# Optimization experiments

Measured on AMD Instinct MI355X. Metric: run time of the kernel, lower is better.

The kernel has to match this reference:

```python
import jax, jax.numpy as jnp
import numpy as np

B, S = 2048, 512
VOCAB, MAXPOS = 50000, 512
DE = 50          # each embedding dim; concat -> 100
DIN, H, OUT = 100, 512, 2


def setup_inputs() -> dict:
    key = jax.random.key(0)
    ks = jax.random.split(key, 12)
    inp = {
        "emb_table": jax.random.normal(ks[0], (VOCAB, DE), jnp.float32) * 0.02,
        "pos_table": jax.random.normal(ks[1], (MAXPOS, DE), jnp.float32) * 0.02,
        "W1": jax.random.normal(ks[2], (DIN, H), jnp.float32) / np.sqrt(DIN),
        "b1": jnp.zeros((H,), jnp.float32),
        "W2": jax.random.normal(ks[3], (H, H), jnp.float32) / np.sqrt(H),
        "b2": jnp.zeros((H,), jnp.float32),
        "W3": jax.random.normal(ks[4], (H, H), jnp.float32) / np.sqrt(H),
        "b3": jnp.zeros((H,), jnp.float32),
        "Wf": jax.random.normal(ks[5], (H, OUT), jnp.float32) / np.sqrt(H),
        "bf": jnp.zeros((OUT,), jnp.float32),
        "seq": jax.random.randint(ks[6], (B, S), 0, VOCAB),
        "seq_length": jax.random.randint(ks[7], (B,), 1, S + 1),  # >=1 to avoid div-by-zero, as in real data
        "pos": jnp.tile(jnp.arange(S, dtype=jnp.int64 if jax.config.jax_enable_x64 else jnp.int32)[None, :], (B, 1)),
    }
    return inp


def reference(emb_table, pos_table, W1, b1, W2, b2, W3, b3, Wf, bf,
              seq, seq_length, pos):
    # Embedding lookups + concat on feature dim -> [B, S, 100]
    x = jnp.concatenate([emb_table[seq], pos_table[pos]], axis=2)
    # Masked mean over the first seq_length[i] tokens (replaces the Python double loop)
    mask = (jnp.arange(S)[None, :] < seq_length[:, None]).astype(x.dtype)  # [B, S]
    pooled = jnp.einsum("bsd,bs->bd", x, mask) / seq_length[:, None].astype(x.dtype)  # [B, 100]
    # MLP stack (Dropout p=0.5 is identity in eval mode)
    h = jax.nn.relu(pooled @ W1 + b1)
    h = jax.nn.relu(h @ W2 + b2)
    h = jax.nn.relu(h @ W3 + b3)
    return h @ Wf + bf  # [B, OUT]
```

## Files before the change

kernel.cpp:

```cpp
#include <hip/hip_runtime.h>

typedef __attribute__((ext_vector_type(8))) short bf16x8;
typedef __attribute__((ext_vector_type(4))) float f32x4;

#define B_    2048
#define S_    512

#define OFF_WF1   0u
#define OFF_WF2   131072u
#define OFF_WF3   655360u
#define OFF_WFF   1179648u
#define OFF_PREF  1196032u
#define OFF_EMBB  1327104u
#define WS_NEED   (OFF_EMBB + 6400000u)

__device__ __forceinline__ unsigned short f2bf(float f) {
    unsigned int u = __float_as_uint(f);
    u += 0x7FFFu + ((u >> 16) & 1u);
    return (unsigned short)(u >> 16);
}

#define MFMA16(a, b, c) __builtin_amdgcn_mfma_f32_16x16x32_bf16((a), (b), (c), 0, 0, 0)

__global__ __launch_bounds__(256) void prep_convert(
    const float* __restrict__ W1, const float* __restrict__ W2,
    const float* __restrict__ W3, const float* __restrict__ Wf,
    const float* __restrict__ post, const int* __restrict__ pos,
    const float* __restrict__ emb,
    unsigned short* __restrict__ ws, float* __restrict__ pref, int do_emb)
{
    const int bid = blockIdx.x;
    const int tid = threadIdx.x;

    if (bid < 152) {
        __shared__ float tile[64][65];
        const float* src; unsigned short* dst;
        int k0, n0, Ksrc, Nsrc, ksTot, nTiles;
        if (bid < 64)       { src=W2; dst=ws+OFF_WF2/2; k0=(bid>>3)*64; n0=(bid&7)*64; Ksrc=512; Nsrc=512; ksTot=16; nTiles=4; }
        else if (bid < 128) { int b=bid-64;  src=W3; dst=ws+OFF_WF3/2; k0=(b>>3)*64; n0=(b&7)*64; Ksrc=512; Nsrc=512; ksTot=16; nTiles=4; }
        else if (bid < 144) { int b=bid-128; src=W1; dst=ws+OFF_WF1/2; k0=(b>>3)*64; n0=(b&7)*64; Ksrc=100; Nsrc=512; ksTot=4;  nTiles=4; }
        else                { int b=bid-144; src=Wf; dst=ws+OFF_WFF/2; k0=b*64;      n0=0;        Ksrc=512; Nsrc=2;   ksTot=16; nTiles=1; }

        const int c  = tid & 63;
        const int r4 = tid >> 6;
#pragma unroll
        for (int rr = 0; rr < 16; ++rr) {
            int r = rr*4 + r4;
            float v = 0.f;
            if (k0 + r < Ksrc && n0 + c < Nsrc) v = src[(size_t)(k0+r)*Nsrc + n0 + c];
            tile[r][c] = v;
        }
        __syncthreads();
        const int nWords = nTiles * 2 * 64;
        for (int w = tid; w < nWords; w += 256) {
            int lane = w & 63, ks_l = (w >> 6) & 1, nt_l = w >> 7;
            int kr = ks_l*32 + ((lane >> 4) << 3);
            int nc = nt_l*16 + (lane & 15);
            uint4 wv;
            wv.x = (unsigned)f2bf(tile[kr+0][nc]) | ((unsigned)f2bf(tile[kr+1][nc]) << 16);
            wv.y = (unsigned)f2bf(tile[kr+2][nc]) | ((unsigned)f2bf(tile[kr+3][nc]) << 16);
            wv.z = (unsigned)f2bf(tile[kr+4][nc]) | ((unsigned)f2bf(tile[kr+5][nc]) << 16);
            wv.w = (unsigned)f2bf(tile[kr+6][nc]) | ((unsigned)f2bf(tile[kr+7][nc]) << 16);
            int ntile = (n0 >> 4) + nt_l, ks = (k0 >> 5) + ks_l;
            ((uint4*)dst)[(size_t)(ntile*ksTot + ks)*64 + lane] = wv;
        }
    } else if (bid == 152) {
        __shared__ int   idx_s[512];
        __shared__ float csum[4][52];
        idx_s[tid]       = pos[tid];
        idx_s[tid + 256] = pos[tid + 256];
        __syncthreads();
        const int c = tid >> 6, d = tid & 63;
        if (d < 50) {
            float run = 0.f;
            for (int b8 = 0; b8 < 16; ++b8) {
                float t[8];
#pragma unroll
                for (int u = 0; u < 8; ++u)
                    t[u] = post[(size_t)idx_s[c*128 + b8*8 + u]*50 + d];
#pragma unroll
                for (int u = 0; u < 8; ++u) {
                    run += t[u];
                    pref[(size_t)(c*128 + b8*8 + u)*64 + d] = run;
                }
            }
            csum[c][d] = run;
        }
        __syncthreads();
        if (d < 50 && c > 0) {
            float off = 0.f;
            for (int cc = 0; cc < c; ++cc) off += csum[cc][d];
            for (int b8 = 0; b8 < 16; ++b8) {
                float t[8];
#pragma unroll
                for (int u = 0; u < 8; ++u)
                    t[u] = pref[(size_t)(c*128 + b8*8 + u)*64 + d];
#pragma unroll
                for (int u = 0; u < 8; ++u)
                    pref[(size_t)(c*128 + b8*8 + u)*64 + d] = t[u] + off;
            }
        }
    } else {
        if (!do_emb) return;
        unsigned* embw = (unsigned*)(ws + OFF_EMBB/2);
        const float2* e2 = (const float2*)emb;
        const unsigned q0 = (unsigned)(bid - 153) * 2048u + (unsigned)tid;
        float2 v[8];
#pragma unroll
        for (int u = 0; u < 8; ++u) {
            unsigned q = q0 + (unsigned)u*256u;
            v[u] = (q < 1250000u) ? e2[q] : (float2){0.f, 0.f};
        }
#pragma unroll
        for (int u = 0; u < 8; ++u) {
            unsigned q = q0 + (unsigned)u*256u;
            if (q < 1250000u) {
                unsigned r = q / 25u, c2 = q - r*25u;
                embw[(size_t)r*32u + c2] =
                    (unsigned)f2bf(v[u].x) | ((unsigned)f2bf(v[u].y) << 16);
            }
        }
    }
}

__device__ __forceinline__ void load_afrags(bf16x8 (&a)[16],
    const unsigned short* h, int row, int kq)
{
#pragma unroll
    for (int ks = 0; ks < 16; ++ks)
        a[ks] = *(const bf16x8*)((const char*)h +
                  (((unsigned)(row * 1024 + ks * 64 + kq * 16)) ^ ((row & 7) << 4)));
}

__device__ __forceinline__ void store_h(unsigned short* h, const f32x4 (&acc)[4],
    const float (&bb)[4], int wave, int row, int kq)
{
#pragma unroll
    for (int nt = 0; nt < 4; ++nt) {
        int c = wave*64 + nt*16 + row;
#pragma unroll
        for (int r4 = 0; r4 < 4; ++r4) {
            int hrow = kq*4 + r4;
            unsigned base = hrow * 1024;
            *(unsigned short*)((char*)h + ((base + c*2) ^ ((hrow & 7) << 4))) =
                f2bf(fmaxf(acc[nt][r4] + bb[nt], 0.f));
        }
    }
}

__device__ __forceinline__ void layer512(
    const bf16x8 (&a)[16], const unsigned short* __restrict__ Wfrag,
    const float* __restrict__ bias, unsigned short* hout,
    int wave, int row, int kq, int lane)
{
    const bf16x8* bp = (const bf16x8*)Wfrag + ((size_t)(wave*4) * 16 * 64) + lane;
    float bb[4];
#pragma unroll
    for (int nt = 0; nt < 4; ++nt) bb[nt] = bias[wave*64 + nt*16 + row];

    bf16x8 bvA[16], bvB[16];
#pragma unroll
    for (int ks = 0; ks < 16; ++ks) bvA[ks] = bp[(0*16 + ks)*64];
#pragma unroll
    for (int ks = 0; ks < 16; ++ks) bvB[ks] = bp[(1*16 + ks)*64];

    f32x4 acc[4];
    acc[0] = (f32x4){0.f,0.f,0.f,0.f};
#pragma unroll
    for (int ks = 0; ks < 16; ++ks) acc[0] = MFMA16(a[ks], bvA[ks], acc[0]);
#pragma unroll
    for (int ks = 0; ks < 16; ++ks) bvA[ks] = bp[(2*16 + ks)*64];

    acc[1] = (f32x4){0.f,0.f,0.f,0.f};
#pragma unroll
    for (int ks = 0; ks < 16; ++ks) acc[1] = MFMA16(a[ks], bvB[ks], acc[1]);
#pragma unroll
    for (int ks = 0; ks < 16; ++ks) bvB[ks] = bp[(3*16 + ks)*64];

    acc[2] = (f32x4){0.f,0.f,0.f,0.f};
#pragma unroll
    for (int ks = 0; ks < 16; ++ks) acc[2] = MFMA16(a[ks], bvA[ks], acc[2]);
    acc[3] = (f32x4){0.f,0.f,0.f,0.f};
#pragma unroll
    for (int ks = 0; ks < 16; ++ks) acc[3] = MFMA16(a[ks], bvB[ks], acc[3]);

    store_h(hout, acc, bb, wave, row, kq);
}

template<int EMODE>
__global__ __launch_bounds__(512, 2) void dan_fused(
    const float* __restrict__ emb, const int* __restrict__ seq,
    const int* __restrict__ seqlen, const unsigned short* __restrict__ ws_ro,
    const float* __restrict__ pref,
    const float* __restrict__ b1, const float* __restrict__ b2,
    const float* __restrict__ b3, const float* __restrict__ bfin,
    float* __restrict__ out)
{
    __shared__ __align__(16) unsigned short idx_s[8*512];
    __shared__ __align__(16) unsigned short pooled_s[16*144];
    __shared__ __align__(16) unsigned short hA[8192];
    __shared__ __align__(16) unsigned short hB[8192];

    const int tid  = threadIdx.x;
    const int wave = tid >> 6;
    const int lane = tid & 63;
    const int row  = lane & 15;
    const int kq   = lane >> 4;
    const int b0   = blockIdx.x * 8;

    const unsigned short* WF1 = ws_ro + OFF_WF1 / 2;
    const unsigned short* WF2 = ws_ro + OFF_WF2 / 2;
    const unsigned short* WF3 = ws_ro + OFF_WF3 / 2;
    const unsigned short* WFF = ws_ro + OFF_WFF / 2;

    for (int i = tid; i < 8*512; i += 512)
        idx_s[i] = (unsigned short)seq[(size_t)b0 * S_ + i];
    for (int i = tid; i < 16*144; i += 512) pooled_s[i] = 0;

    bf16x8 w1f[4][4];
    {
        const bf16x8* bp1 = (const bf16x8*)WF1 + ((size_t)(wave*4) * 4 * 64) + lane;
#pragma unroll
        for (int ci = 0; ci < 4; ++ci)
#pragma unroll
            for (int ks = 0; ks < 4; ++ks) w1f[ci][ks] = bp1[(ci*4 + ks)*64];
    }
    __syncthreads();

    const int L = seqlen[b0 + wave];
    const float Lf = (float)L;
    const unsigned short* idxr = idx_s + wave * 512;

    if (EMODE == 0) {
        const int tg = lane >> 3, dq = lane & 7;
        const uint4* tbl = (const uint4*)(ws_ro + OFF_EMBB / 2);
        float acc8[8];
#pragma unroll
        for (int j = 0; j < 8; ++j) acc8[j] = 0.f;

        const int Lfull = L & ~63;
        for (int s0 = 0; s0 < Lfull; s0 += 64) {
            uint4 q[8];
#pragma unroll
            for (int u = 0; u < 8; ++u) {
                int tok = idxr[s0 + u*8 + tg];
                q[u] = tbl[(size_t)tok * 8 + dq];
            }
#pragma unroll
            for (int u = 0; u < 8; ++u) {
                unsigned dw[4] = {q[u].x, q[u].y, q[u].z, q[u].w};
#pragma unroll
                for (int v = 0; v < 4; ++v) {
                    acc8[2*v]   += __uint_as_float(dw[v] << 16);
                    acc8[2*v+1] += __uint_as_float(dw[v] & 0xffff0000u);
                }
            }
        }
        for (int s0 = Lfull; s0 < L; s0 += 8) {
            int s = s0 + tg;
            uint4 q = {0u,0u,0u,0u};
            if (s < L) q = tbl[(size_t)idxr[s] * 8 + dq];
            unsigned dw[4] = {q.x, q.y, q.z, q.w};
#pragma unroll
            for (int v = 0; v < 4; ++v) {
                acc8[2*v]   += __uint_as_float(dw[v] << 16);
                acc8[2*v+1] += __uint_as_float(dw[v] & 0xffff0000u);
            }
        }
#pragma unroll
        for (int j = 0; j < 8; ++j) acc8[j] += __shfl_xor(acc8[j], 8);
#pragma unroll
        for (int j = 0; j < 8; ++j) acc8[j] += __shfl_xor(acc8[j], 16);
#pragma unroll
        for (int j = 0; j < 8; ++j) acc8[j] += __shfl_xor(acc8[j], 32);
        if (lane < 8) {
#pragma unroll
            for (int j = 0; j < 8; ++j) {
                int d = lane*8 + j;
                if (d < 50) pooled_s[wave*144 + d] = f2bf(acc8[j] / Lf);
            }
        }
    } else {
        float accE = 0.f;
        for (int s = 0; s < L; ++s) {
            int tok = idxr[s];
            if (lane < 50) accE += emb[(size_t)tok*50 + lane];
        }
        if (lane < 50) pooled_s[wave*144 + lane] = f2bf(accE / Lf);
    }
    if (lane < 50)
        pooled_s[wave*144 + 50 + lane] = f2bf(pref[(size_t)(L-1)*64 + lane] / Lf);
    __syncthreads();

    {
        bf16x8 a1[4];
#pragma unroll
        for (int ks = 0; ks < 4; ++ks)
            a1[ks] = *(const bf16x8*)&pooled_s[row*144 + ks*32 + kq*8];
        f32x4 acc[4];
        float bb[4];
#pragma unroll
        for (int ci = 0; ci < 4; ++ci) {
            bb[ci] = b1[wave*64 + ci*16 + row];
            acc[ci] = (f32x4){0.f,0.f,0.f,0.f};
#pragma unroll
            for (int ks = 0; ks < 4; ++ks) acc[ci] = MFMA16(a1[ks], w1f[ci][ks], acc[ci]);
        }
        store_h(hA, acc, bb, wave, row, kq);
    }
    __syncthreads();

    bf16x8 a[16];
    load_afrags(a, hA, row, kq);
    layer512(a, WF2, b2, hB, wave, row, kq, lane);
    __syncthreads();

    load_afrags(a, hB, row, kq);
    layer512(a, WF3, b3, hA, wave, row, kq, lane);
    __syncthreads();

    if (wave == 0) {
        load_afrags(a, hA, row, kq);
        const bf16x8* bpf = (const bf16x8*)WFF + lane;
        f32x4 accf = {0.f, 0.f, 0.f, 0.f};
#pragma unroll
        for (int ks = 0; ks < 16; ++ks) {
            bf16x8 bv = bpf[ks*64];
            accf = MFMA16(a[ks], bv, accf);
        }
        if (row < 2 && kq < 2) {
            float bb = bfin[row];
#pragma unroll
            for (int r4 = 0; r4 < 4; ++r4) {
                int m = kq*4 + r4;
                out[(size_t)(b0 + m) * 2 + row] = accf[r4] + bb;
            }
        }
    }
}

extern "C" void kernel_launch(void* const* d_in, const int* in_sizes, int n_in,
                              void* d_out, int out_size, void* d_ws, size_t ws_size,
                              hipStream_t stream)
{
    const float* emb    = (const float*)d_in[0];
    const float* post   = (const float*)d_in[1];
    const float* W1     = (const float*)d_in[2];
    const float* b1     = (const float*)d_in[3];
    const float* W2     = (const float*)d_in[4];
    const float* b2     = (const float*)d_in[5];
    const float* W3     = (const float*)d_in[6];
    const float* b3     = (const float*)d_in[7];
    const float* Wf     = (const float*)d_in[8];
    const float* bf     = (const float*)d_in[9];
    const int*   seq    = (const int*)d_in[10];
    const int*   seqlen = (const int*)d_in[11];
    const int*   pos    = (const int*)d_in[12];
    float*       out    = (float*)d_out;

    unsigned short* ws = (unsigned short*)d_ws;
    float* pref = (float*)((char*)d_ws + OFF_PREF);
    const int do_emb = (ws_size >= (size_t)WS_NEED) ? 1 : 0;

    const int prep_blocks = do_emb ? (153 + 611) : 153;
    prep_convert<<<prep_blocks, 256, 0, stream>>>(W1, W2, W3, Wf, post, pos, emb,
                                                  ws, pref, do_emb);
    if (do_emb)
        dan_fused<0><<<B_ / 8, 512, 0, stream>>>(emb, seq, seqlen, ws, pref,
                                                 b1, b2, b3, bf, out);
    else
        dan_fused<1><<<B_ / 8, 512, 0, stream>>>(emb, seq, seqlen, ws, pref,
                                                 b1, b2, b3, bf, out);
}
```

Before: 44.13 us.

## Split embedding pooling into its own kernel ahead of MLP kernel

Moves the gather-and-mean pooling out of the fused MLP kernel into a separate pool_kernel with 4 rows per 256-thread block (512 blocks), writing bf16 pooled rows to a global workspace buffer. The gather loop is rewritten as a software-pipelined loop that keeps four loads in flight, and the MLP kernel now only reads the pooled rows. The aim is to raise occupancy and memory-level parallelism for the latency-bound gather, which was previously limited by the heavy MLP kernel's resources and its per-block imbalance from varying sequence lengths. In exchange it adds an extra kernel launch and a global round trip for the pooled activations.

```diff
diff --git a/kernel.cpp b/kernel.cpp
--- a/kernel.cpp
+++ b/kernel.cpp
@@ -11,7 +11,8 @@
 #define OFF_WF3   655360u
 #define OFF_WFF   1179648u
 #define OFF_PREF  1196032u
-#define OFF_EMBB  1327104u
+#define OFF_POOLG 1327104u
+#define OFF_EMBB  1851392u
 #define WS_NEED   (OFF_EMBB + 6400000u)
 
 __device__ __forceinline__ unsigned short f2bf(float f) {
@@ -123,6 +124,88 @@
     }
 }
 
+__device__ __forceinline__ void acc_uint4(float (&a)[8], uint4 q) {
+    unsigned dw[4] = {q.x, q.y, q.z, q.w};
+#pragma unroll
+    for (int v = 0; v < 4; ++v) {
+        a[2*v]   += __uint_as_float(dw[v] << 16);
+        a[2*v+1] += __uint_as_float(dw[v] & 0xffff0000u);
+    }
+}
+
+#define LOADQ(qv, bidx) { int s_ = (bidx)*8 + tg; qv = (uint4){0u,0u,0u,0u}; \
+    if (s_ < L) qv = tbl[(size_t)idxr[s_]*8u + (unsigned)dq]; }
+
+template<int EMODE>
+__global__ __launch_bounds__(256) void pool_kernel(
+    const float* __restrict__ emb, const int* __restrict__ seq,
+    const int* __restrict__ seqlen, const unsigned short* __restrict__ ws_ro,
+    const float* __restrict__ pref, unsigned short* __restrict__ pooled_g)
+{
+    __shared__ unsigned short idx_s[4*512];
+    const int tid = threadIdx.x, wave = tid >> 6, lane = tid & 63;
+    const int b0 = blockIdx.x * 4;
+    for (int i = tid; i < 4*512; i += 256)
+        idx_s[i] = (unsigned short)seq[(size_t)b0 * S_ + i];
+    __syncthreads();
+
+    const int row = b0 + wave;
+    const int L = seqlen[row];
+    const float invL = 1.f / (float)L;
+    const unsigned short* idxr = idx_s + wave*512;
+
+    if (EMODE == 0) {
+        const int tg = lane >> 3, dq = lane & 7;
+        const uint4* tbl = (const uint4*)(ws_ro + OFF_EMBB/2);
+        float acc8[8] = {0.f,0.f,0.f,0.f,0.f,0.f,0.f,0.f};
+        uint4 q0, q1, q2, q3;
+        LOADQ(q0, 0) LOADQ(q1, 1) LOADQ(q2, 2) LOADQ(q3, 3)
+        const int nbr = (L + 7) >> 3;
+        for (int i = 0; i < nbr; i += 4) {
+            acc_uint4(acc8, q0); LOADQ(q0, i+4)
+            acc_uint4(acc8, q1); LOADQ(q1, i+5)
+            acc_uint4(acc8, q2); LOADQ(q2, i+6)
+            acc_uint4(acc8, q3); LOADQ(q3, i+7)
+        }
+#pragma unroll
+        for (int j = 0; j < 8; ++j) acc8[j] += __shfl_xor(acc8[j], 8);
+#pragma unroll
+        for (int j = 0; j < 8; ++j) acc8[j] += __shfl_xor(acc8[j], 16);
+#pragma unroll
+        for (int j = 0; j < 8; ++j) acc8[j] += __shfl_xor(acc8[j], 32);
+        if (lane < 16) {
+            const float* prow = pref + (size_t)(L-1)*64;
+            unsigned short w8[8];
+#pragma unroll
+            for (int j = 0; j < 8; ++j) {
+                int d = lane*8 + j;
+                float v;
+                if (d < 50)       v = acc8[j] * invL;
+                else if (d < 100) v = prow[d - 50] * invL;
+                else              v = 0.f;
+                w8[j] = f2bf(v);
+            }
+            bf16x8 wv;
+#pragma unroll
+            for (int j = 0; j < 8; ++j) wv[j] = (short)w8[j];
+            ((bf16x8*)pooled_g)[(size_t)row*16 + lane] = wv;
+        }
+    } else {
+        float accE = 0.f;
+        for (int s = 0; s < L; ++s) {
+            int tok = idxr[s];
+            if (lane < 50) accE += emb[(size_t)tok*50 + lane];
+        }
+        if (lane < 50)  pooled_g[(size_t)row*128 + lane] = f2bf(accE * invL);
+        else if (lane < 64) pooled_g[(size_t)row*128 + lane + 64] = 0;
+        if (lane < 50)
+            pooled_g[(size_t)row*128 + 50 + lane] =
+                f2bf(pref[(size_t)(L-1)*64 + lane] * invL);
+        else if (lane < 64)
+            pooled_g[(size_t)row*128 + (lane - 50 >= 0 ? 0 : 0) + 100 + (lane - 50)] = 0;
+    }
+}
+
 __device__ __forceinline__ void load_afrags(bf16x8 (&a)[16],
     const unsigned short* h, int row, int kq)
 {
@@ -187,16 +270,12 @@
     store_h(hout, acc, bb, wave, row, kq);
 }
 
-template<int EMODE>
-__global__ __launch_bounds__(512, 2) void dan_fused(
-    const float* __restrict__ emb, const int* __restrict__ seq,
-    const int* __restrict__ seqlen, const unsigned short* __restrict__ ws_ro,
-    const float* __restrict__ pref,
+__global__ __launch_bounds__(512, 2) void dan_mlp(
+    const unsigned short* __restrict__ ws_ro,
     const float* __restrict__ b1, const float* __restrict__ b2,
     const float* __restrict__ b3, const float* __restrict__ bfin,
     float* __restrict__ out)
 {
-    __shared__ __align__(16) unsigned short idx_s[8*512];
     __shared__ __align__(16) unsigned short pooled_s[16*144];
     __shared__ __align__(16) unsigned short hA[8192];
     __shared__ __align__(16) unsigned short hB[8192];
@@ -212,10 +291,7 @@
     const unsigned short* WF2 = ws_ro + OFF_WF2 / 2;
     const unsigned short* WF3 = ws_ro + OFF_WF3 / 2;
     const unsigned short* WFF = ws_ro + OFF_WFF / 2;
-
-    for (int i = tid; i < 8*512; i += 512)
-        idx_s[i] = (unsigned short)seq[(size_t)b0 * S_ + i];
-    for (int i = tid; i < 16*144; i += 512) pooled_s[i] = 0;
+    const unsigned short* pooled_g = ws_ro + OFF_POOLG / 2;
 
     bf16x8 w1f[4][4];
     {
@@ -225,71 +301,13 @@
 #pragma unroll
             for (int ks = 0; ks < 4; ++ks) w1f[ci][ks] = bp1[(ci*4 + ks)*64];
     }
-    __syncthreads();
-
-    const int L = seqlen[b0 + wave];
-    const float Lf = (float)L;
-    const unsigned short* idxr = idx_s + wave * 512;
-
-    if (EMODE == 0) {
-        const int tg = lane >> 3, dq = lane & 7;
-        const uint4* tbl = (const uint4*)(ws_ro + OFF_EMBB / 2);
-        float acc8[8];
-#pragma unroll
-        for (int j = 0; j < 8; ++j) acc8[j] = 0.f;
-
-        const int Lfull = L & ~63;
-        for (int s0 = 0; s0 < Lfull; s0 += 64) {
-            uint4 q[8];
-#pragma unroll
-            for (int u = 0; u < 8; ++u) {
-                int tok = idxr[s0 + u*8 + tg];
-                q[u] = tbl[(size_t)tok * 8 + dq];
-            }
-#pragma unroll
-            for (int u = 0; u < 8; ++u) {
-                unsigned dw[4] = {q[u].x, q[u].y, q[u].z, q[u].w};
-#pragma unroll
-                for (int v = 0; v < 4; ++v) {
-                    acc8[2*v]   += __uint_as_float(dw[v] << 16);
-                    acc8[2*v+1] += __uint_as_float(dw[v] & 0xffff0000u);
-                }
-            }
-        }
-        for (int s0 = Lfull; s0 < L; s0 += 8) {
-            int s = s0 + tg;
-            uint4 q = {0u,0u,0u,0u};
-            if (s < L) q = tbl[(size_t)idxr[s] * 8 + dq];
-            unsigned dw[4] = {q.x, q.y, q.z, q.w};
-#pragma unroll
-            for (int v = 0; v < 4; ++v) {
-                acc8[2*v]   += __uint_as_float(dw[v] << 16);
-                acc8[2*v+1] += __uint_as_float(dw[v] & 0xffff0000u);
-            }
-        }
-#pragma unroll
-        for (int j = 0; j < 8; ++j) acc8[j] += __shfl_xor(acc8[j], 8);
-#pragma unroll
-        for (int j = 0; j < 8; ++j) acc8[j] += __shfl_xor(acc8[j], 16);
-#pragma unroll
-        for (int j = 0; j < 8; ++j) acc8[j] += __shfl_xor(acc8[j], 32);
-        if (lane < 8) {
-#pragma unroll
-            for (int j = 0; j < 8; ++j) {
-                int d = lane*8 + j;
-                if (d < 50) pooled_s[wave*144 + d] = f2bf(acc8[j] / Lf);
-            }
-        }
-    } else {
-        float accE = 0.f;
-        for (int s = 0; s < L; ++s) {
-            int tok = idxr[s];
-            if (lane < 50) accE += emb[(size_t)tok*50 + lane];
-        }
-        if (lane < 50) pooled_s[wave*144 + lane] = f2bf(accE / Lf);
-    }
-    if (lane < 50)
-        pooled_s[wave*144 + 50 + lane] = f2bf(pref[(size_t)(L-1)*64 + lane] / Lf);
+
+    for (int i = tid; i < 16*144; i += 512) {
+        int r = i / 144, c = i - r*144;
+        unsigned short v = 0;
+        if (r < 8 && c < 128) v = pooled_g[(size_t)(b0 + r)*128 + c];
+        pooled_s[i] = v;
+    }
     __syncthreads();
 
     {
@@ -360,15 +378,15 @@
 
     unsigned short* ws = (unsigned short*)d_ws;
     float* pref = (float*)((char*)d_ws + OFF_PREF);
+    unsigned short* pooled_g = ws + OFF_POOLG/2;
     const int do_emb = (ws_size >= (size_t)WS_NEED) ? 1 : 0;
 
     const int prep_blocks = do_emb ? (153 + 611) : 153;
     prep_convert<<<prep_blocks, 256, 0, stream>>>(W1, W2, W3, Wf, post, pos, emb,
                                                   ws, pref, do_emb);
     if (do_emb)
-        dan_fused<0><<<B_ / 8, 512, 0, stream>>>(emb, seq, seqlen, ws, pref,
-                                                 b1, b2, b3, bf, out);
+        pool_kernel<0><<<512, 256, 0, stream>>>(emb, seq, seqlen, ws, pref, pooled_g);
     else
-        dan_fused<1><<<B_ / 8, 512, 0, stream>>>(emb, seq, seqlen, ws, pref,
-                                                 b1, b2, b3, bf, out);
-}
+        pool_kernel<1><<<512, 256, 0, stream>>>(emb, seq, seqlen, ws, pref, pooled_g);
+    dan_mlp<<<B_ / 8, 512, 0, stream>>>(ws, b1, b2, b3, bf, out);
+}
```

New measurement: 57.09 us. 29.4% more time.
